# Kernel tuning notes

Hardware: AMD Instinct MI355X
Metric: run time of the kernel (lower is better)

The kernel has to match this reference:

```python
import jax, jax.numpy as jnp
import numpy as np

E, D_MODEL, D_FF = 8, 1024, 4096
B, S = 4, 2048


def setup_inputs() -> dict:
    key = jax.random.key(0)
    ks = jax.random.split(key, 7)
    scale_in = 1.0 / np.sqrt(D_MODEL)
    scale_ff = 1.0 / np.sqrt(D_FF)
    return {
        "x": jax.random.normal(ks[0], (B, S, D_MODEL), dtype=jnp.float32),
        "w1": jax.random.normal(ks[1], (E, D_MODEL, D_FF), dtype=jnp.float32) * scale_in,
        "b1": jax.random.normal(ks[2], (E, D_FF), dtype=jnp.float32) * 0.01,
        "w2": jax.random.normal(ks[3], (E, D_FF, D_MODEL), dtype=jnp.float32) * scale_ff,
        "b2": jax.random.normal(ks[4], (E, D_MODEL), dtype=jnp.float32) * 0.01,
        "gate_w": jax.random.normal(ks[5], (D_MODEL, E), dtype=jnp.float32) * scale_in,
        "gate_b": jax.random.normal(ks[6], (E,), dtype=jnp.float32) * 0.01,
    }


def reference(x, w1, b1, w2, b2, gate_w, gate_b):
    # Gating: softmax then top-1 (argmax of probs == argmax of logits)
    gate_logits = x @ gate_w + gate_b                      # [B,S,E]
    gate_probs = jax.nn.softmax(gate_logits, axis=-1)
    top1 = jnp.argmax(gate_probs, axis=-1)                 # [B,S] int
    mask = jax.nn.one_hot(top1, E, dtype=x.dtype)          # [B,S,E]

    # Dense compute of every expert on every token (faithful to source)
    h = jax.nn.relu(jnp.einsum('bsd,edf->ebsf', x, w1) + b1[:, None, None, :])  # [E,B,S,F]
    y = jnp.einsum('ebsf,efd->ebsd', h, w2) + b2[:, None, None, :]              # [E,B,S,D]

    # Top-1 mask-and-sum combine (note: no gate-prob scaling in the original)
    out = jnp.einsum('ebsd,bse->bsd', y, mask)             # [B,S,D]
    return out
```

## Files before the change

kernel.cpp:

```cpp
#include <hip/hip_runtime.h>
#include <stdint.h>

#define DM 1024
#define DF 4096
#define NE 8
#define NTOK 8192
#define MT128 72
#define MT256 40

typedef __attribute__((ext_vector_type(8))) short short8;
typedef __attribute__((ext_vector_type(8))) unsigned short ushort8v;
typedef __attribute__((ext_vector_type(4))) float floatx4;

__device__ inline unsigned short f2bf(float f) {
    union { float f; unsigned u; } v; v.f = f;
    unsigned u = v.u;
    u += 0x7fffu + ((u >> 16) & 1u);
    return (unsigned short)(u >> 16);
}

#define GLDS(g, l) __builtin_amdgcn_global_load_lds( \
    (const __attribute__((address_space(1))) void*)(g), \
    (__attribute__((address_space(3))) void*)(l), 16, 0, 0)

#define VMW(N)  asm volatile("s_waitcnt vmcnt(" #N ")" ::: "memory")
#define LGKM0   asm volatile("s_waitcnt lgkmcnt(0)" ::: "memory")
#define SCHED0  __builtin_amdgcn_sched_barrier(0)
#define BAR     __builtin_amdgcn_s_barrier()

__global__ void gate_kernel(const float* __restrict__ x, const float* __restrict__ gw,
                            const float* __restrict__ gb, int* __restrict__ top1,
                            unsigned short* __restrict__ xb) {
    int t = blockIdx.x;
    int lane = threadIdx.x;
    const float* xr = x + (size_t)t * DM;
    unsigned short* xbr = xb + (size_t)t * DM;
    double acc[NE];
#pragma unroll
    for (int e = 0; e < NE; ++e) acc[e] = 0.0;
    for (int j = 0; j < DM / 64; ++j) {
        int d = j * 64 + lane;
        float xf = xr[d];
        xbr[d] = f2bf(xf);
        double xv = (double)xf;
        const float* g = gw + (size_t)d * NE;
#pragma unroll
        for (int e = 0; e < NE; ++e) acc[e] = fma(xv, (double)g[e], acc[e]);
    }
#pragma unroll
    for (int e = 0; e < NE; ++e) {
        for (int off = 32; off > 0; off >>= 1)
            acc[e] += __shfl_down(acc[e], off, 64);
    }
    if (lane == 0) {
        int best = 0;
        double bv = acc[0] + (double)gb[0];
        for (int e = 1; e < NE; ++e) {
            double v = acc[e] + (double)gb[e];
            if (v > bv) { bv = v; best = e; }
        }
        top1[t] = best;
    }
}

__global__ void count_kernel(const int* __restrict__ top1, int* __restrict__ ctrl) {
    int t = blockIdx.x * 256 + threadIdx.x;
    int e = top1[t];
    int lane = threadIdx.x & 63;
#pragma unroll
    for (int ex = 0; ex < NE; ++ex) {
        unsigned long long m = __ballot(e == ex);
        if (m != 0ull && lane == (__ffsll((long long)m) - 1))
            atomicAdd(&ctrl[ex], __popcll(m));
    }
}

__global__ void prefix_kernel(int* ctrl) {
    if (threadIdx.x == 0) {
        int s = 0, t256 = 0, t128 = 0;
        for (int e = 0; e < NE; ++e) {
            int cnt = ctrl[e];
            ctrl[8 + e] = s; ctrl[17 + e] = s;
            for (int m = 0; m * 256 < cnt; ++m) {
                ctrl[32 + 3 * t256] = e;
                ctrl[33 + 3 * t256] = s + m * 256;
                int rr = cnt - m * 256;
                ctrl[34 + 3 * t256] = rr < 256 ? rr : 256;
                ++t256;
            }
            for (int m = 0; m * 128 < cnt; ++m) {
                ctrl[160 + 3 * t128] = e;
                ctrl[161 + 3 * t128] = s + m * 128;
                int rr = cnt - m * 128;
                ctrl[162 + 3 * t128] = rr < 128 ? rr : 128;
                ++t128;
            }
            s += cnt;
        }
        ctrl[16] = s;
        ctrl[25] = t256;
        ctrl[26] = t128;
    }
}

__global__ void scatter_kernel(const int* __restrict__ top1, int* __restrict__ ctrl,
                               int* __restrict__ perm) {
    int t = blockIdx.x * 256 + threadIdx.x;
    int e = top1[t];
    int lane = threadIdx.x & 63;
#pragma unroll
    for (int ex = 0; ex < NE; ++ex) {
        unsigned long long m = __ballot(e == ex);
        if (m == 0ull) continue;
        int leader = __ffsll((long long)m) - 1;
        int base = 0;
        if (lane == leader) base = atomicAdd(&ctrl[17 + ex], __popcll(m));
        base = __shfl(base, leader, 64);
        if (e == ex) {
            int pos = __popcll(m & ((1ull << lane) - 1ull));
            perm[base + pos] = t;
        }
    }
}

__global__ void transpose_bf16(const float* __restrict__ src, unsigned short* __restrict__ dst,
                               int R, int C) {
    __shared__ float tile[64][65];
    int tilesR = R >> 6, tilesC = C >> 6;
    int bid = blockIdx.x;
    int e = bid / (tilesR * tilesC);
    int rem = bid % (tilesR * tilesC);
    int tr = rem / tilesC, tc = rem % tilesC;
    const float* s = src + (size_t)e * R * C + (size_t)(tr * 64) * C + tc * 64;
    unsigned short* d = dst + (size_t)e * R * C + (size_t)(tc * 64) * R + tr * 64;
    int tid = threadIdx.x;
#pragma unroll
    for (int i = 0; i < 4; ++i) {
        int idx = i * 256 + tid;
        int r = idx >> 4, c4 = (idx & 15) * 4;
        float4 v = *(const float4*)(s + (size_t)r * C + c4);
        tile[r][c4 + 0] = v.x; tile[r][c4 + 1] = v.y;
        tile[r][c4 + 2] = v.z; tile[r][c4 + 3] = v.w;
    }
    __syncthreads();
#pragma unroll
    for (int i = 0; i < 2; ++i) {
        int idx = i * 256 + tid;
        int c = idx >> 3, r8 = (idx & 7) * 8;
        ushort8v o;
#pragma unroll
        for (int j = 0; j < 8; ++j) o[j] = f2bf(tile[r8 + j][c]);
        *(ushort8v*)(d + (size_t)c * R + r8) = o;
    }
}

#define F1_SLAB(u, SU, STG, W) do { \
    if (STG) { \
        int kk_ = ((SU) + 3) * 32; \
        GLDS(ap0 + kk_, &As[((u) + 3) & 3][(size_t)tid * 8]); \
        GLDS(ap1 + kk_, &As[((u) + 3) & 3][(size_t)(512 + tid) * 8]); \
        GLDS(bp0 + kk_, &Bs[((u) + 3) & 3][(size_t)tid * 8]); \
        GLDS(bp1 + kk_, &Bs[((u) + 3) & 3][(size_t)(512 + tid) * 8]); \
    } \
    short8 af[8], bf[4]; \
    _Pragma("unroll") \
    for (int m_ = 0; m_ < 8; ++m_) af[m_] = *(const short8*)&As[u][aoff[m_]]; \
    _Pragma("unroll") \
    for (int n_ = 0; n_ < 4; ++n_) bf[n_] = *(const short8*)&Bs[u][boff[n_]]; \
    LGKM0; SCHED0; \
    __builtin_amdgcn_s_setprio(1); \
    _Pragma("unroll") \
    for (int m_ = 0; m_ < 8; ++m_) \
        _Pragma("unroll") \
        for (int n_ = 0; n_ < 4; ++n_) \
            acc[m_][n_] = __builtin_amdgcn_mfma_f32_16x16x32_bf16(af[m_], bf[n_], acc[m_][n_], 0, 0, 0); \
    __builtin_amdgcn_s_setprio(0); \
    W; SCHED0; BAR; \
} while (0)

__global__ __launch_bounds__(512, 2) void ffn1_gemm(
    const unsigned short* __restrict__ A,
    const unsigned short* __restrict__ Bt,
    const float* __restrict__ bias,
    const int* __restrict__ ctrl,
    const int* __restrict__ perm,
    unsigned short* __restrict__ Hout) {
    constexpr int K = DM;
    constexpr int N = DF;
    constexpr int NT = N / 256;
    constexpr int NKI = K / 32;
    constexpr int SLABSZ = 256 * 32;
    constexpr int G = 8;

    int nwg = gridDim.x;
    int bo = blockIdx.x;
    int q = nwg >> 3, r = nwg & 7;
    int xcd = bo & 7, lid = bo >> 3;
    int b = (xcd < r ? xcd * (q + 1) : r * (q + 1) + (xcd - r) * q) + lid;

    int grp = b / (G * NT);
    int ii = b % (G * NT);
    int nt = ii / G;
    int til = grp * G + (ii % G);
    if (til >= ctrl[25]) return;
    int e       = ctrl[32 + 3 * til];
    int rowbase = ctrl[33 + 3 * til];
    int rows    = ctrl[34 + 3 * til];

    __shared__ __align__(16) unsigned short As[4][SLABSZ];
    __shared__ __align__(16) unsigned short Bs[4][SLABSZ];

    int tid = threadIdx.x, lane = tid & 63, wave = tid >> 6;
    int wm = (wave >> 2) * 128;
    int wn = (wave & 3) * 64;

    int rA0 = tid >> 2, rA1 = 128 + (tid >> 2);
    int kofs = ((tid & 3) ^ ((tid >> 3) & 3)) * 8;
    int c0 = rowbase + (rA0 < rows ? rA0 : rows - 1);
    int c1 = rowbase + (rA1 < rows ? rA1 : rows - 1);
    const unsigned short* ap0 = A + (size_t)perm[c0] * K + kofs;
    const unsigned short* ap1 = A + (size_t)perm[c1] * K + kofs;
    const unsigned short* bb  = Bt + (size_t)e * N * K + (size_t)(nt * 256) * K + kofs;
    const unsigned short* bp0 = bb + (size_t)rA0 * K;
    const unsigned short* bp1 = bb + (size_t)rA1 * K;

    int aoff[8], boff[4];
#pragma unroll
    for (int m = 0; m < 8; ++m) {
        int R = wm + m * 16 + (lane & 15);
        aoff[m] = R * 32 + (((lane >> 4) ^ ((R >> 1) & 3)) * 8);
    }
#pragma unroll
    for (int n = 0; n < 4; ++n) {
        int R = wn + n * 16 + (lane & 15);
        boff[n] = R * 32 + (((lane >> 4) ^ ((R >> 1) & 3)) * 8);
    }

    floatx4 acc[8][4];
#pragma unroll
    for (int i = 0; i < 8; ++i)
#pragma unroll
        for (int j = 0; j < 4; ++j) acc[i][j] = floatx4{0.f, 0.f, 0.f, 0.f};

#pragma unroll
    for (int s = 0; s < 3; ++s) {
        GLDS(ap0 + s * 32, &As[s][(size_t)tid * 8]);
        GLDS(ap1 + s * 32, &As[s][(size_t)(512 + tid) * 8]);
        GLDS(bp0 + s * 32, &Bs[s][(size_t)tid * 8]);
        GLDS(bp1 + s * 32, &Bs[s][(size_t)(512 + tid) * 8]);
    }
    VMW(8); SCHED0; BAR;

#pragma unroll 1
    for (int s = 0; s < NKI - 4; s += 4) {
        F1_SLAB(0, s + 0, 1, VMW(8));
        F1_SLAB(1, s + 1, 1, VMW(8));
        F1_SLAB(2, s + 2, 1, VMW(8));
        F1_SLAB(3, s + 3, 1, VMW(8));
    }
    F1_SLAB(0, NKI - 4, 1, VMW(8));
    F1_SLAB(1, NKI - 3, 0, VMW(4));
    F1_SLAB(2, NKI - 2, 0, VMW(0));
    F1_SLAB(3, NKI - 1, 0, (void)0);

    int col0 = nt * 256 + wn + (lane & 15);
    int rowq = (lane >> 4) * 4;
    float bv[4];
#pragma unroll
    for (int n = 0; n < 4; ++n) bv[n] = bias[e * N + col0 + n * 16];

#pragma unroll
    for (int m = 0; m < 8; ++m) {
#pragma unroll
        for (int r2 = 0; r2 < 4; ++r2) {
            int lr = wm + m * 16 + rowq + r2;
            if (lr < rows) {
                unsigned short* hr = Hout + (size_t)(rowbase + lr) * DF + col0;
#pragma unroll
                for (int n = 0; n < 4; ++n) {
                    float v = acc[m][n][r2] + bv[n];
                    v = v > 0.f ? v : 0.f;
                    hr[n * 16] = f2bf(v);
                }
            }
        }
    }
}
#undef F1_SLAB

__global__ __launch_bounds__(256) void ffn2_gemm(
    const unsigned short* __restrict__ A,
    const unsigned short* __restrict__ Bt,
    const float* __restrict__ bias,
    const int* __restrict__ ctrl,
    const int* __restrict__ perm,
    float* __restrict__ Yout) {
    constexpr int K = DF;
    constexpr int N = DM;
    constexpr int NT = N / 128;
    constexpr int G = 8;
    constexpr int NKI = K / 64;

    int nwg = gridDim.x;
    int bo = blockIdx.x;
    int q = nwg >> 3, r = nwg & 7;
    int xcd = bo & 7, lid = bo >> 3;
    int b = (xcd < r ? xcd * (q + 1) : r * (q + 1) + (xcd - r) * q) + lid;

    int grp = b / (G * NT);
    int ii = b % (G * NT);
    int nt = ii / G;
    int til = grp * G + (ii % G);
    if (til >= ctrl[26]) return;
    int e       = ctrl[160 + 3 * til];
    int rowbase = ctrl[161 + 3 * til];
    int rows    = ctrl[162 + 3 * til];

    __shared__ __align__(16) unsigned short As[2][128 * 64];
    __shared__ __align__(16) unsigned short Bs[2][128 * 64];

    int tid = threadIdx.x;
    int lane = tid & 63;
    int wave = tid >> 6;
    int wm = (wave & 1) * 64;
    int wn = (wave >> 1) * 64;

    const unsigned short* arow[4];
    const unsigned short* brow[4];
    const unsigned short* bbase = Bt + (size_t)e * N * K + (size_t)(nt * 128) * K;
#pragma unroll
    for (int i = 0; i < 4; ++i) {
        int c = i * 256 + tid;
        int rr2 = c >> 3;
        int gk = (c & 7) ^ (rr2 & 7);
        int rr = rr2 < rows ? rr2 : rows - 1;
        arow[i] = A + (size_t)(rowbase + rr) * K + gk * 8;
        brow[i] = bbase + (size_t)rr2 * K + gk * 8;
    }

    floatx4 acc[4][4];
#pragma unroll
    for (int i = 0; i < 4; ++i)
#pragma unroll
        for (int j = 0; j < 4; ++j) acc[i][j] = floatx4{0.f, 0.f, 0.f, 0.f};

#define F2_STAGE(BUF, KK) do { \
    _Pragma("unroll") \
    for (int i_ = 0; i_ < 4; ++i_) { \
        GLDS(arow[i_] + (KK), &As[BUF][(i_ * 256 + tid) * 8]); \
        GLDS(brow[i_] + (KK), &Bs[BUF][(i_ * 256 + tid) * 8]); \
    } } while (0)

#define F2_COMPUTE(BUF) do { \
    _Pragma("unroll") \
    for (int ks_ = 0; ks_ < 2; ++ks_) { \
        short8 af[4], bfr[4]; \
        _Pragma("unroll") \
        for (int m_ = 0; m_ < 4; ++m_) { \
            int R_ = wm + m_ * 16 + (lane & 15); \
            int s_ = (ks_ * 4 + (lane >> 4)) ^ (R_ & 7); \
            af[m_] = *(const short8*)&As[BUF][R_ * 64 + s_ * 8]; \
        } \
        _Pragma("unroll") \
        for (int n_ = 0; n_ < 4; ++n_) { \
            int R_ = wn + n_ * 16 + (lane & 15); \
            int s_ = (ks_ * 4 + (lane >> 4)) ^ (R_ & 7); \
            bfr[n_] = *(const short8*)&Bs[BUF][R_ * 64 + s_ * 8]; \
        } \
        _Pragma("unroll") \
        for (int m_ = 0; m_ < 4; ++m_) \
            _Pragma("unroll") \
            for (int n_ = 0; n_ < 4; ++n_) \
                acc[m_][n_] = __builtin_amdgcn_mfma_f32_16x16x32_bf16(af[m_], bfr[n_], acc[m_][n_], 0, 0, 0); \
    } } while (0)

    F2_STAGE(0, 0);
    __syncthreads();
#pragma unroll 1
    for (int t = 0; t < NKI; t += 2) {
        int kk = t * 64;
        F2_STAGE(1, kk + 64);
        F2_COMPUTE(0);
        __syncthreads();
        if (t + 2 < NKI) F2_STAGE(0, kk + 128);
        F2_COMPUTE(1);
        __syncthreads();
    }
#undef F2_STAGE
#undef F2_COMPUTE

    int col0 = nt * 128 + wn + (lane & 15);
    int rowq = (lane >> 4) * 4;
    float bv[4];
#pragma unroll
    for (int n = 0; n < 4; ++n) bv[n] = bias[e * N + col0 + n * 16];

#pragma unroll
    for (int m = 0; m < 4; ++m) {
#pragma unroll
        for (int r2 = 0; r2 < 4; ++r2) {
            int lr = wm + m * 16 + rowq + r2;
            if (lr < rows) {
                float* yr = Yout + (size_t)perm[rowbase + lr] * DM + col0;
#pragma unroll
                for (int n = 0; n < 4; ++n)
                    yr[n * 16] = acc[m][n][r2] + bv[n];
            }
        }
    }
}

extern "C" void kernel_launch(void* const* d_in, const int* in_sizes, int n_in,
                              void* d_out, int out_size, void* d_ws, size_t ws_size,
                              hipStream_t stream) {
    const float* x  = (const float*)d_in[0];
    const float* w1 = (const float*)d_in[1];
    const float* b1 = (const float*)d_in[2];
    const float* w2 = (const float*)d_in[3];
    const float* b2 = (const float*)d_in[4];
    const float* gw = (const float*)d_in[5];
    const float* gb = (const float*)d_in[6];
    float* out = (float*)d_out;

    char* ws = (char*)d_ws;
    int* ctrl = (int*)ws;
    int* top1 = (int*)(ws + 2048);
    int* perm = (int*)(ws + 2048 + 32768);
    size_t o = 67584;
    unsigned short* xb  = (unsigned short*)(ws + o);        o += (size_t)NTOK * DM * 2;
    unsigned short* w1t = (unsigned short*)(ws + o);        o += (size_t)NE * DM * DF * 2;
    unsigned short* w2t = (unsigned short*)(ws + o);        o += (size_t)NE * DM * DF * 2;
    unsigned short* H   = (unsigned short*)(ws + o);

    hipMemsetAsync(ctrl, 0, 2048, stream);
    gate_kernel<<<NTOK, 64, 0, stream>>>(x, gw, gb, top1, xb);
    count_kernel<<<NTOK / 256, 256, 0, stream>>>(top1, ctrl);
    prefix_kernel<<<1, 64, 0, stream>>>(ctrl);
    scatter_kernel<<<NTOK / 256, 256, 0, stream>>>(top1, ctrl, perm);
    transpose_bf16<<<NE * (DM / 64) * (DF / 64), 256, 0, stream>>>(w1, w1t, DM, DF);
    transpose_bf16<<<NE * (DF / 64) * (DM / 64), 256, 0, stream>>>(w2, w2t, DF, DM);
    ffn1_gemm<<<MT256 * (DF / 256), 512, 0, stream>>>(xb, w1t, b1, ctrl, perm, H);
    ffn2_gemm<<<MT128 * (DM / 128), 256, 0, stream>>>(H, w2t, b2, ctrl, perm, out);
}
```

Measured before the change: 625.8 us.

## Reuse 256x256 pipelined GEMM template for FFN2 and merge weight transposes

Replaces the separate 128x128 double-buffered FFN2 kernel with a templated version of the FFN1 256x256 tile, 4-stage global_load_lds pipeline, so the second GEMM gets larger tiles, deeper prefetch and more data reuse. FFN2 reads H rows contiguously and scatters fp32 outputs through perm. The two weight-transpose launches are also fused into one launch. The risk is fewer workgroups for FFN2 (40x4 tiles), which may underfill the GPU's compute units.

Result: faster. 585.8 us (-6.4%).

```diff
diff --git a/kernel.cpp b/kernel.cpp
--- a/kernel.cpp
+++ b/kernel.cpp
@@ -5,7 +5,6 @@
 #define DF 4096
 #define NE 8
 #define NTOK 8192
-#define MT128 72
 #define MT256 40
 
 typedef __attribute__((ext_vector_type(8))) short short8;
@@ -77,7 +76,7 @@
 
 __global__ void prefix_kernel(int* ctrl) {
     if (threadIdx.x == 0) {
-        int s = 0, t256 = 0, t128 = 0;
+        int s = 0, t256 = 0;
         for (int e = 0; e < NE; ++e) {
             int cnt = ctrl[e];
             ctrl[8 + e] = s; ctrl[17 + e] = s;
@@ -88,18 +87,10 @@
                 ctrl[34 + 3 * t256] = rr < 256 ? rr : 256;
                 ++t256;
             }
-            for (int m = 0; m * 128 < cnt; ++m) {
-                ctrl[160 + 3 * t128] = e;
-                ctrl[161 + 3 * t128] = s + m * 128;
-                int rr = cnt - m * 128;
-                ctrl[162 + 3 * t128] = rr < 128 ? rr : 128;
-                ++t128;
-            }
             s += cnt;
         }
         ctrl[16] = s;
         ctrl[25] = t256;
-        ctrl[26] = t128;
     }
 }
 
@@ -123,11 +114,15 @@
     }
 }
 
-__global__ void transpose_bf16(const float* __restrict__ src, unsigned short* __restrict__ dst,
-                               int R, int C) {
+__global__ void transpose_both(const float* __restrict__ w1, unsigned short* __restrict__ w1t,
+                               const float* __restrict__ w2, unsigned short* __restrict__ w2t) {
+    constexpr int NT1 = NE * (DM / 64) * (DF / 64);
     __shared__ float tile[64][65];
+    int bid = blockIdx.x;
+    const float* src; unsigned short* dst; int R, C;
+    if (bid < NT1) { src = w1; dst = w1t; R = DM; C = DF; }
+    else           { bid -= NT1; src = w2; dst = w2t; R = DF; C = DM; }
     int tilesR = R >> 6, tilesC = C >> 6;
-    int bid = blockIdx.x;
     int e = bid / (tilesR * tilesC);
     int rem = bid % (tilesR * tilesC);
     int tr = rem / tilesC, tc = rem % tilesC;
@@ -154,7 +149,7 @@
     }
 }
 
-#define F1_SLAB(u, SU, STG, W) do { \
+#define F_SLAB(u, SU, STG, W) do { \
     if (STG) { \
         int kk_ = ((SU) + 3) * 32; \
         GLDS(ap0 + kk_, &As[((u) + 3) & 3][(size_t)tid * 8]); \
@@ -178,15 +173,17 @@
     W; SCHED0; BAR; \
 } while (0)
 
-__global__ __launch_bounds__(512, 2) void ffn1_gemm(
+template<bool FFN1>
+__global__ __launch_bounds__(512, 2) void ffn_gemm(
     const unsigned short* __restrict__ A,
     const unsigned short* __restrict__ Bt,
     const float* __restrict__ bias,
     const int* __restrict__ ctrl,
     const int* __restrict__ perm,
-    unsigned short* __restrict__ Hout) {
-    constexpr int K = DM;
-    constexpr int N = DF;
+    unsigned short* __restrict__ Hout,
+    float* __restrict__ Yout) {
+    constexpr int K = FFN1 ? DM : DF;
+    constexpr int N = FFN1 ? DF : DM;
     constexpr int NT = N / 256;
     constexpr int NKI = K / 32;
     constexpr int SLABSZ = 256 * 32;
@@ -218,8 +215,15 @@
     int kofs = ((tid & 3) ^ ((tid >> 3) & 3)) * 8;
     int c0 = rowbase + (rA0 < rows ? rA0 : rows - 1);
     int c1 = rowbase + (rA1 < rows ? rA1 : rows - 1);
-    const unsigned short* ap0 = A + (size_t)perm[c0] * K + kofs;
-    const unsigned short* ap1 = A + (size_t)perm[c1] * K + kofs;
+    const unsigned short* ap0;
+    const unsigned short* ap1;
+    if (FFN1) {
+        ap0 = A + (size_t)perm[c0] * K + kofs;
+        ap1 = A + (size_t)perm[c1] * K + kofs;
+    } else {
+        ap0 = A + (size_t)c0 * K + kofs;
+        ap1 = A + (size_t)c1 * K + kofs;
+    }
     const unsigned short* bb  = Bt + (size_t)e * N * K + (size_t)(nt * 256) * K + kofs;
     const unsigned short* bp0 = bb + (size_t)rA0 * K;
     const unsigned short* bp1 = bb + (size_t)rA1 * K;
@@ -253,15 +257,15 @@
 
 #pragma unroll 1
     for (int s = 0; s < NKI - 4; s += 4) {
-        F1_SLAB(0, s + 0, 1, VMW(8));
-        F1_SLAB(1, s + 1, 1, VMW(8));
-        F1_SLAB(2, s + 2, 1, VMW(8));
-        F1_SLAB(3, s + 3, 1, VMW(8));
-    }
-    F1_SLAB(0, NKI - 4, 1, VMW(8));
-    F1_SLAB(1, NKI - 3, 0, VMW(4));
-    F1_SLAB(2, NKI - 2, 0, VMW(0));
-    F1_SLAB(3, NKI - 1, 0, (void)0);
+        F_SLAB(0, s + 0, 1, VMW(8));
+        F_SLAB(1, s + 1, 1, VMW(8));
+        F_SLAB(2, s + 2, 1, VMW(8));
+        F_SLAB(3, s + 3, 1, VMW(8));
+    }
+    F_SLAB(0, NKI - 4, 1, VMW(8));
+    F_SLAB(1, NKI - 3, 0, VMW(4));
+    F_SLAB(2, NKI - 2, 0, VMW(0));
+    F_SLAB(3, NKI - 1, 0, (void)0);
 
     int col0 = nt * 256 + wn + (lane & 15);
     int rowq = (lane >> 4) * 4;
@@ -275,140 +279,25 @@
         for (int r2 = 0; r2 < 4; ++r2) {
             int lr = wm + m * 16 + rowq + r2;
             if (lr < rows) {
-                unsigned short* hr = Hout + (size_t)(rowbase + lr) * DF + col0;
-#pragma unroll
-                for (int n = 0; n < 4; ++n) {
-                    float v = acc[m][n][r2] + bv[n];
-                    v = v > 0.f ? v : 0.f;
-                    hr[n * 16] = f2bf(v);
+                if (FFN1) {
+                    unsigned short* hr = Hout + (size_t)(rowbase + lr) * DF + col0;
+#pragma unroll
+                    for (int n = 0; n < 4; ++n) {
+                        float v = acc[m][n][r2] + bv[n];
+                        v = v > 0.f ? v : 0.f;
+                        hr[n * 16] = f2bf(v);
+                    }
+                } else {
+                    float* yr = Yout + (size_t)perm[rowbase + lr] * DM + col0;
+#pragma unroll
+                    for (int n = 0; n < 4; ++n)
+                        yr[n * 16] = acc[m][n][r2] + bv[n];
                 }
             }
         }
     }
 }
-#undef F1_SLAB
-
-__global__ __launch_bounds__(256) void ffn2_gemm(
-    const unsigned short* __restrict__ A,
-    const unsigned short* __restrict__ Bt,
-    const float* __restrict__ bias,
-    const int* __restrict__ ctrl,
-    const int* __restrict__ perm,
-    float* __restrict__ Yout) {
-    constexpr int K = DF;
-    constexpr int N = DM;
-    constexpr int NT = N / 128;
-    constexpr int G = 8;
-    constexpr int NKI = K / 64;
-
-    int nwg = gridDim.x;
-    int bo = blockIdx.x;
-    int q = nwg >> 3, r = nwg & 7;
-    int xcd = bo & 7, lid = bo >> 3;
-    int b = (xcd < r ? xcd * (q + 1) : r * (q + 1) + (xcd - r) * q) + lid;
-
-    int grp = b / (G * NT);
-    int ii = b % (G * NT);
-    int nt = ii / G;
-    int til = grp * G + (ii % G);
-    if (til >= ctrl[26]) return;
-    int e       = ctrl[160 + 3 * til];
-    int rowbase = ctrl[161 + 3 * til];
-    int rows    = ctrl[162 + 3 * til];
-
-    __shared__ __align__(16) unsigned short As[2][128 * 64];
-    __shared__ __align__(16) unsigned short Bs[2][128 * 64];
-
-    int tid = threadIdx.x;
-    int lane = tid & 63;
-    int wave = tid >> 6;
-    int wm = (wave & 1) * 64;
-    int wn = (wave >> 1) * 64;
-
-    const unsigned short* arow[4];
-    const unsigned short* brow[4];
-    const unsigned short* bbase = Bt + (size_t)e * N * K + (size_t)(nt * 128) * K;
-#pragma unroll
-    for (int i = 0; i < 4; ++i) {
-        int c = i * 256 + tid;
-        int rr2 = c >> 3;
-        int gk = (c & 7) ^ (rr2 & 7);
-        int rr = rr2 < rows ? rr2 : rows - 1;
-        arow[i] = A + (size_t)(rowbase + rr) * K + gk * 8;
-        brow[i] = bbase + (size_t)rr2 * K + gk * 8;
-    }
-
-    floatx4 acc[4][4];
-#pragma unroll
-    for (int i = 0; i < 4; ++i)
-#pragma unroll
-        for (int j = 0; j < 4; ++j) acc[i][j] = floatx4{0.f, 0.f, 0.f, 0.f};
-
-#define F2_STAGE(BUF, KK) do { \
-    _Pragma("unroll") \
-    for (int i_ = 0; i_ < 4; ++i_) { \
-        GLDS(arow[i_] + (KK), &As[BUF][(i_ * 256 + tid) * 8]); \
-        GLDS(brow[i_] + (KK), &Bs[BUF][(i_ * 256 + tid) * 8]); \
-    } } while (0)
-
-#define F2_COMPUTE(BUF) do { \
-    _Pragma("unroll") \
-    for (int ks_ = 0; ks_ < 2; ++ks_) { \
-        short8 af[4], bfr[4]; \
-        _Pragma("unroll") \
-        for (int m_ = 0; m_ < 4; ++m_) { \
-            int R_ = wm + m_ * 16 + (lane & 15); \
-            int s_ = (ks_ * 4 + (lane >> 4)) ^ (R_ & 7); \
-            af[m_] = *(const short8*)&As[BUF][R_ * 64 + s_ * 8]; \
-        } \
-        _Pragma("unroll") \
-        for (int n_ = 0; n_ < 4; ++n_) { \
-            int R_ = wn + n_ * 16 + (lane & 15); \
-            int s_ = (ks_ * 4 + (lane >> 4)) ^ (R_ & 7); \
-            bfr[n_] = *(const short8*)&Bs[BUF][R_ * 64 + s_ * 8]; \
-        } \
-        _Pragma("unroll") \
-        for (int m_ = 0; m_ < 4; ++m_) \
-            _Pragma("unroll") \
-            for (int n_ = 0; n_ < 4; ++n_) \
-                acc[m_][n_] = __builtin_amdgcn_mfma_f32_16x16x32_bf16(af[m_], bfr[n_], acc[m_][n_], 0, 0, 0); \
-    } } while (0)
-
-    F2_STAGE(0, 0);
-    __syncthreads();
-#pragma unroll 1
-    for (int t = 0; t < NKI; t += 2) {
-        int kk = t * 64;
-        F2_STAGE(1, kk + 64);
-        F2_COMPUTE(0);
-        __syncthreads();
-        if (t + 2 < NKI) F2_STAGE(0, kk + 128);
-        F2_COMPUTE(1);
-        __syncthreads();
-    }
-#undef F2_STAGE
-#undef F2_COMPUTE
-
-    int col0 = nt * 128 + wn + (lane & 15);
-    int rowq = (lane >> 4) * 4;
-    float bv[4];
-#pragma unroll
-    for (int n = 0; n < 4; ++n) bv[n] = bias[e * N + col0 + n * 16];
-
-#pragma unroll
-    for (int m = 0; m < 4; ++m) {
-#pragma unroll
-        for (int r2 = 0; r2 < 4; ++r2) {
-            int lr = wm + m * 16 + rowq + r2;
-            if (lr < rows) {
-                float* yr = Yout + (size_t)perm[rowbase + lr] * DM + col0;
-#pragma unroll
-                for (int n = 0; n < 4; ++n)
-                    yr[n * 16] = acc[m][n][r2] + bv[n];
-            }
-        }
-    }
-}
+#undef F_SLAB
 
 extern "C" void kernel_launch(void* const* d_in, const int* in_sizes, int n_in,
                               void* d_out, int out_size, void* d_ws, size_t ws_size,
@@ -437,8 +326,7 @@
     count_kernel<<<NTOK / 256, 256, 0, stream>>>(top1, ctrl);
     prefix_kernel<<<1, 64, 0, stream>>>(ctrl);
     scatter_kernel<<<NTOK / 256, 256, 0, stream>>>(top1, ctrl, perm);
-    transpose_bf16<<<NE * (DM / 64) * (DF / 64), 256, 0, stream>>>(w1, w1t, DM, DF);
-    transpose_bf16<<<NE * (DF / 64) * (DM / 64), 256, 0, stream>>>(w2, w2t, DF, DM);
-    ffn1_gemm<<<MT256 * (DF / 256), 512, 0, stream>>>(xb, w1t, b1, ctrl, perm, H);
-    ffn2_gemm<<<MT128 * (DM / 128), 256, 0, stream>>>(H, w2t, b2, ctrl, perm, out);
-}
+    transpose_both<<<2 * NE * (DM / 64) * (DF / 64), 256, 0, stream>>>(w1, w1t, w2, w2t);
+    ffn_gemm<true ><<<MT256 * (DF / 256), 512, 0, stream>>>(xb, w1t, b1, ctrl, perm, H, nullptr);
+    ffn_gemm<false><<<MT256 * (DM / 256), 512, 0, stream>>>(H, w2t, b2, ctrl, perm, nullptr, out);
+}
```
